# Kernel tuning notes

Measured on AMD Instinct MI355X. Metric: run time of the kernel, lower is better.

Reference implementation:

```python
import jax, jax.numpy as jnp
import numpy as np

THRESHOLD = 0.95
B, T, H = 32, 2000, 512
NUM_TARGETS = 250.0  # alphas normalized so each row sums to this (mimics alpha *= num/_num)
MAX_LABEL_LEN = 256


def setup_inputs() -> dict:
    key = jax.random.key(0)
    k1, k2 = jax.random.split(key)
    hidden = jax.random.normal(k1, (B, T, H), dtype=jnp.float32)
    u = jax.random.uniform(k2, (B, T), dtype=jnp.float32)
    alphas = u / u.sum(-1, keepdims=True) * NUM_TARGETS  # per-row sum == NUM_TARGETS
    return {"hidden": hidden, "alphas": alphas, "max_label_len": MAX_LABEL_LEN}


def _cif(hidden, alphas, max_label_len, threshold=THRESHOLD):
    """Continuous integrate-and-fire: sequential scan over time + fire-gather."""
    Bn, Tn, Hn = hidden.shape

    def step(carry, inp):
        integrate, frame = carry              # [B], [B, H]
        alpha, h = inp                        # [B], [B, H]
        dist_completion = 1.0 - integrate
        integ = integrate + alpha
        fire = integ > threshold              # [B] bool
        cur = jnp.where(fire, dist_completion, alpha)
        remainds = alpha - cur
        frame_out = frame + cur[:, None] * h  # emitted frame at this step
        integ_next = jnp.where(fire, integ - 1.0, integ)
        frame_next = jnp.where(fire[:, None], remainds[:, None] * h, frame_out)
        return (integ_next, frame_next), (integ, frame_out)

    init = (jnp.zeros((Bn,), hidden.dtype), jnp.zeros((Bn, Hn), hidden.dtype))
    xs = (jnp.swapaxes(alphas, 0, 1), jnp.swapaxes(hidden, 0, 1))  # time-major
    _, (fires_t, frames_t) = jax.lax.scan(step, init, xs)
    fires = jnp.swapaxes(fires_t, 0, 1)    # [B, T]
    frames = jnp.swapaxes(frames_t, 0, 1)  # [B, T, H]

    # Gather fired frames per batch row, left-packed and zero-padded to max_label_len.
    mask = fires > threshold                               # [B, T]
    pos = jnp.cumsum(mask.astype(jnp.int32), axis=1) - 1   # running fire index
    pos = jnp.where(mask, pos, max_label_len)              # non-fires go to dump slot
    out = jnp.zeros((Bn, max_label_len + 1, Hn), hidden.dtype)
    out = out.at[jnp.arange(Bn)[:, None], pos].set(frames)
    return out[:, :max_label_len]  # drop dump slot -> [B, L, H]


def reference(hidden, alphas, max_label_len):
    return _cif(hidden, alphas, max_label_len)
```

## Files before the change

### kernel.cpp

```cpp
#include <hip/hip_runtime.h>
#include <stdint.h>

static constexpr int   Bn      = 32;
static constexpr int   Tn      = 2000;
static constexpr int   Hn      = 512;
static constexpr int   Ln      = 256;
static constexpr float kThresh = 0.95f;
static constexpr int   TCHUNK  = 40;
static constexpr int   NTCH    = Tn / TCHUNK;
static constexpr int   CSPLIT  = 2;
static constexpr int   MSTRIDE = 64;
static constexpr unsigned PUBF = 0x40000000u;

__global__ __launch_bounds__(64, 1) void cif_fused_kernel(
    const float* __restrict__ hidden,
    const float* __restrict__ alphas,
    uint64_t* __restrict__ meta,
    float* __restrict__ out) {
  const int lane = threadIdx.x;
  __shared__ __align__(16) float alds[Tn + 64];

  if (blockIdx.x < Bn) {
    __builtin_amdgcn_s_setprio(3);
    const int b = blockIdx.x;
    {
      const float4* __restrict__ arow =
          reinterpret_cast<const float4*>(alphas + (size_t)b * Tn);
      for (int i = lane; i < Tn / 4; i += 64)
        *reinterpret_cast<float4*>(&alds[4 * i]) = arow[i];
      for (int i = Tn / 4 + lane; i < (Tn + 64) / 4; i += 64)
        *reinterpret_cast<float4*>(&alds[4 * i]) =
            make_float4(0.f, 0.f, 0.f, 0.f);
    }
    __syncthreads();

    const float4* __restrict__ lds4 =
        reinterpret_cast<const float4*>(&alds[0]);
    float I  = 0.0f;
    int   fc = 0;

    float4 q0 = lds4[0], q1 = lds4[1], q2 = lds4[2], q3 = lds4[3],
           q4 = lds4[4];
    int rd = 5;

    auto step4 = [&](const float4& q) {
#pragma unroll
      for (int j = 0; j < 4; ++j) {
        const float a = (j == 0) ? q.x : (j == 1) ? q.y : (j == 2) ? q.z : q.w;
        const float integ = I + a;
        const bool  fire  = integ > kThresh;
        I  = fire ? (integ - 1.0f) : integ;
        fc += fire ? 1 : 0;
      }
    };

    for (int c = 0; c < 100; ++c) {
      if (lane == 0 && (c & 1) == 0) {
        const uint64_t v = ((uint64_t)__float_as_uint(I) << 32) |
                           (uint64_t)(PUBF | (unsigned)fc);
        __hip_atomic_store(&meta[(size_t)b * MSTRIDE + (c >> 1)], v,
                           __ATOMIC_RELAXED, __HIP_MEMORY_SCOPE_AGENT);
      }
      step4(q0); q0 = lds4[rd + 0];
      step4(q1); q1 = lds4[rd + 1];
      step4(q2); q2 = lds4[rd + 2];
      step4(q3); q3 = lds4[rd + 3];
      step4(q4); q4 = lds4[rd + 4];
      rd += 5;
    }
    return;
  }

  const int idx  = blockIdx.x - Bn;
  const int b    = idx & (Bn - 1);
  const int q    = idx >> 5;
  const int tc   = q >> 1;
  const int half = q & 1;
  const int t_start = tc * TCHUNK;
  const int col  = half * (Hn / CSPLIT) + lane * 4;

  auto wait_meta = [&](int c) -> uint64_t {
    const uint64_t* p = &meta[(size_t)b * MSTRIDE + c];
    uint64_t v;
    for (;;) {
      v = __hip_atomic_load(p, __ATOMIC_RELAXED, __HIP_MEMORY_SCOPE_AGENT);
      if ((unsigned)v & PUBF) break;
      __builtin_amdgcn_s_sleep(16);
    }
    return v;
  };

  const float* __restrict__ arow = alphas + (size_t)b * Tn;

  float I; int s;
  if (tc == 0) { I = 0.0f; s = 0; }
  else {
    const uint64_t v = wait_meta(tc);
    I = __uint_as_float((unsigned)(v >> 32));
    s = (int)((unsigned)v & 0xFFFFu);
  }

  int   t_prev   = -1;
  float rem_prev = 0.0f;
  for (int k = 1; tc - k >= 0 && t_prev < 0; ++k) {
    const int ck = tc - k;
    float Ik;
    if (ck == 0) Ik = 0.0f;
    else {
      const uint64_t v = wait_meta(ck);
      Ik = __uint_as_float((unsigned)(v >> 32));
    }
    const float* __restrict__ ap = arow + ck * TCHUNK;
    int lt = -1; float lrem = 0.0f;
#pragma unroll
    for (int j = 0; j < TCHUNK; ++j) {
      const float a     = ap[j];
      const float integ = Ik + a;
      const bool  fire  = integ > kThresh;
      if (fire) { lt = ck * TCHUNK + j; lrem = a - (1.0f - Ik); }
      Ik = fire ? (integ - 1.0f) : integ;
    }
    if (lt >= 0) { t_prev = lt; rem_prev = lrem; }
  }

  const float* __restrict__ hb = hidden + (size_t)b * Tn * Hn + col;
  float4 acc = make_float4(0.f, 0.f, 0.f, 0.f);

  auto loadh = [&](int t) -> float4 {
    return *reinterpret_cast<const float4*>(hb + (size_t)t * Hn);
  };

  if (t_prev >= 0) {
    const float4 h = loadh(t_prev);
    acc.x = rem_prev * h.x; acc.y = rem_prev * h.y;
    acc.z = rem_prev * h.z; acc.w = rem_prev * h.w;
  }
  for (int t = t_prev + 1; t < t_start; ++t) {
    const float a  = arow[t];
    const float4 h = loadh(t);
    acc.x += a * h.x; acc.y += a * h.y;
    acc.z += a * h.z; acc.w += a * h.w;
  }

  float4 hc = loadh(t_start);
  for (int j = 0; j < TCHUNK; ++j) {
    const int t  = t_start + j;
    const int tn = (j + 1 < TCHUNK) ? t + 1 : t;
    const float4 hn = loadh(tn);
    const float a     = arow[t];
    const float integ = I + a;
    const bool  fire  = integ > kThresh;
    if (fire) {
      const float cw = 1.0f - I;
      acc.x += cw * hc.x; acc.y += cw * hc.y;
      acc.z += cw * hc.z; acc.w += cw * hc.w;
      if (s < Ln) {
        float* op = out + ((size_t)b * Ln + s) * Hn + col;
        *reinterpret_cast<float4*>(op) = acc;
      }
      const float rem = a - cw;
      acc.x = rem * hc.x; acc.y = rem * hc.y;
      acc.z = rem * hc.z; acc.w = rem * hc.w;
      s += 1;
      I  = integ - 1.0f;
    } else {
      acc.x += a * hc.x; acc.y += a * hc.y;
      acc.z += a * hc.z; acc.w += a * hc.w;
      I = integ;
    }
    hc = hn;
  }
  if (tc == NTCH - 1) {
    const float4 z = make_float4(0.f, 0.f, 0.f, 0.f);
    for (int s2 = s; s2 < Ln; ++s2) {
      float* op = out + ((size_t)b * Ln + s2) * Hn + col;
      *reinterpret_cast<float4*>(op) = z;
    }
  }
}

extern "C" void kernel_launch(void* const* d_in, const int* in_sizes, int n_in,
                              void* d_out, int out_size, void* d_ws, size_t ws_size,
                              hipStream_t stream) {
  const float* hidden = (const float*)d_in[0];
  const float* alphas = (const float*)d_in[1];
  float* out = (float*)d_out;

  uint64_t* meta = (uint64_t*)d_ws;
  hipMemsetAsync(meta, 0, (size_t)Bn * MSTRIDE * sizeof(uint64_t), stream);

  const int nblocks = Bn + NTCH * Bn * CSPLIT;
  cif_fused_kernel<<<nblocks, 64, 0, stream>>>(hidden, alphas, meta, out);
}
```

Measured before the change: 56.43 us.

## Split hidden columns four ways and deepen prefetch of hidden rows

```diff
diff --git a/kernel.cpp b/kernel.cpp
--- a/kernel.cpp
+++ b/kernel.cpp
@@ -8,7 +8,7 @@
 static constexpr float kThresh = 0.95f;
 static constexpr int   TCHUNK  = 40;
 static constexpr int   NTCH    = Tn / TCHUNK;
-static constexpr int   CSPLIT  = 2;
+static constexpr int   CSPLIT  = 4;
 static constexpr int   MSTRIDE = 64;
 static constexpr unsigned PUBF = 0x40000000u;
 
@@ -74,10 +74,10 @@
   const int idx  = blockIdx.x - Bn;
   const int b    = idx & (Bn - 1);
   const int q    = idx >> 5;
-  const int tc   = q >> 1;
-  const int half = q & 1;
+  const int tc   = q >> 2;
+  const int quar = q & 3;
   const int t_start = tc * TCHUNK;
-  const int col  = half * (Hn / CSPLIT) + lane * 4;
+  const int col  = quar * (Hn / CSPLIT) + lane * 2;
 
   auto wait_meta = [&](int c) -> uint64_t {
     const uint64_t* p = &meta[(size_t)b * MSTRIDE + c];
@@ -124,57 +124,55 @@
   }
 
   const float* __restrict__ hb = hidden + (size_t)b * Tn * Hn + col;
-  float4 acc = make_float4(0.f, 0.f, 0.f, 0.f);
+  float2 acc = make_float2(0.f, 0.f);
 
-  auto loadh = [&](int t) -> float4 {
-    return *reinterpret_cast<const float4*>(hb + (size_t)t * Hn);
+  auto loadh = [&](int t) -> float2 {
+    return *reinterpret_cast<const float2*>(hb + (size_t)t * Hn);
   };
 
   if (t_prev >= 0) {
-    const float4 h = loadh(t_prev);
+    const float2 h = loadh(t_prev);
     acc.x = rem_prev * h.x; acc.y = rem_prev * h.y;
-    acc.z = rem_prev * h.z; acc.w = rem_prev * h.w;
   }
   for (int t = t_prev + 1; t < t_start; ++t) {
     const float a  = arow[t];
-    const float4 h = loadh(t);
+    const float2 h = loadh(t);
     acc.x += a * h.x; acc.y += a * h.y;
-    acc.z += a * h.z; acc.w += a * h.w;
   }
 
-  float4 hc = loadh(t_start);
+  float2 p0 = loadh(t_start);
+  float2 p1 = loadh(t_start + 1);
+  float2 p2 = loadh(t_start + 2);
+  float2 p3 = loadh(t_start + 3);
   for (int j = 0; j < TCHUNK; ++j) {
-    const int t  = t_start + j;
-    const int tn = (j + 1 < TCHUNK) ? t + 1 : t;
-    const float4 hn = loadh(tn);
+    const int t   = t_start + j;
+    const int tpf = t_start + ((j + 4 < TCHUNK) ? j + 4 : TCHUNK - 1);
+    const float2 pn = loadh(tpf);
     const float a     = arow[t];
     const float integ = I + a;
     const bool  fire  = integ > kThresh;
     if (fire) {
       const float cw = 1.0f - I;
-      acc.x += cw * hc.x; acc.y += cw * hc.y;
-      acc.z += cw * hc.z; acc.w += cw * hc.w;
+      acc.x += cw * p0.x; acc.y += cw * p0.y;
       if (s < Ln) {
         float* op = out + ((size_t)b * Ln + s) * Hn + col;
-        *reinterpret_cast<float4*>(op) = acc;
+        *reinterpret_cast<float2*>(op) = acc;
       }
       const float rem = a - cw;
-      acc.x = rem * hc.x; acc.y = rem * hc.y;
-      acc.z = rem * hc.z; acc.w = rem * hc.w;
+      acc.x = rem * p0.x; acc.y = rem * p0.y;
       s += 1;
       I  = integ - 1.0f;
     } else {
-      acc.x += a * hc.x; acc.y += a * hc.y;
-      acc.z += a * hc.z; acc.w += a * hc.w;
+      acc.x += a * p0.x; acc.y += a * p0.y;
       I = integ;
     }
-    hc = hn;
+    p0 = p1; p1 = p2; p2 = p3; p3 = pn;
   }
   if (tc == NTCH - 1) {
-    const float4 z = make_float4(0.f, 0.f, 0.f, 0.f);
+    const float2 z = make_float2(0.f, 0.f);
     for (int s2 = s; s2 < Ln; ++s2) {
       float* op = out + ((size_t)b * Ln + s2) * Hn + col;
-      *reinterpret_cast<float4*>(op) = z;
+      *reinterpret_cast<float2*>(op) = z;
     }
   }
 }
```

Result: no change. 56.71 us (+0.5%).

## Publish last-fire position per chunk and skip trailing non-firing work

Applied to the files above, without the earlier changes.

```diff
diff --git a/kernel.cpp b/kernel.cpp
--- a/kernel.cpp
+++ b/kernel.cpp
@@ -16,6 +16,7 @@
     const float* __restrict__ hidden,
     const float* __restrict__ alphas,
     uint64_t* __restrict__ meta,
+    uint64_t* __restrict__ meta2,
     float* __restrict__ out) {
   const int lane = threadIdx.x;
   __shared__ __align__(16) float alds[Tn + 64];
@@ -36,19 +37,24 @@
 
     const float4* __restrict__ lds4 =
         reinterpret_cast<const float4*>(&alds[0]);
-    float I  = 0.0f;
-    int   fc = 0;
+    float I       = 0.0f;
+    int   fc      = 0;
+    int   lastT1  = 0;
+    float lastRem = 0.0f;
 
     float4 q0 = lds4[0], q1 = lds4[1], q2 = lds4[2], q3 = lds4[3],
            q4 = lds4[4];
     int rd = 5;
 
-    auto step4 = [&](const float4& q) {
+    auto step4 = [&](const float4& q, int tbase) {
 #pragma unroll
       for (int j = 0; j < 4; ++j) {
         const float a = (j == 0) ? q.x : (j == 1) ? q.y : (j == 2) ? q.z : q.w;
         const float integ = I + a;
         const bool  fire  = integ > kThresh;
+        const float cw    = 1.0f - I;
+        lastT1  = fire ? (tbase + j + 1) : lastT1;
+        lastRem = fire ? (a - cw) : lastRem;
         I  = fire ? (integ - 1.0f) : integ;
         fc += fire ? 1 : 0;
       }
@@ -56,16 +62,21 @@
 
     for (int c = 0; c < 100; ++c) {
       if (lane == 0 && (c & 1) == 0) {
-        const uint64_t v = ((uint64_t)__float_as_uint(I) << 32) |
-                           (uint64_t)(PUBF | (unsigned)fc);
-        __hip_atomic_store(&meta[(size_t)b * MSTRIDE + (c >> 1)], v,
+        const uint64_t v1 = ((uint64_t)__float_as_uint(I) << 32) |
+                            (uint64_t)(PUBF | (unsigned)fc);
+        __hip_atomic_store(&meta[(size_t)b * MSTRIDE + (c >> 1)], v1,
+                           __ATOMIC_RELAXED, __HIP_MEMORY_SCOPE_AGENT);
+        const uint64_t v2 = ((uint64_t)__float_as_uint(lastRem) << 32) |
+                            (uint64_t)(PUBF | (unsigned)lastT1);
+        __hip_atomic_store(&meta2[(size_t)b * MSTRIDE + (c >> 1)], v2,
                            __ATOMIC_RELAXED, __HIP_MEMORY_SCOPE_AGENT);
       }
-      step4(q0); q0 = lds4[rd + 0];
-      step4(q1); q1 = lds4[rd + 1];
-      step4(q2); q2 = lds4[rd + 2];
-      step4(q3); q3 = lds4[rd + 3];
-      step4(q4); q4 = lds4[rd + 4];
+      const int t0 = c * 20;
+      step4(q0, t0);      q0 = lds4[rd + 0];
+      step4(q1, t0 + 4);  q1 = lds4[rd + 1];
+      step4(q2, t0 + 8);  q2 = lds4[rd + 2];
+      step4(q3, t0 + 12); q3 = lds4[rd + 3];
+      step4(q4, t0 + 16); q4 = lds4[rd + 4];
       rd += 5;
     }
     return;
@@ -79,8 +90,8 @@
   const int t_start = tc * TCHUNK;
   const int col  = half * (Hn / CSPLIT) + lane * 4;
 
-  auto wait_meta = [&](int c) -> uint64_t {
-    const uint64_t* p = &meta[(size_t)b * MSTRIDE + c];
+  auto wait64 = [&](uint64_t* arr, int c) -> uint64_t {
+    const uint64_t* p = &arr[(size_t)b * MSTRIDE + c];
     uint64_t v;
     for (;;) {
       v = __hip_atomic_load(p, __ATOMIC_RELAXED, __HIP_MEMORY_SCOPE_AGENT);
@@ -95,41 +106,50 @@
   float I; int s;
   if (tc == 0) { I = 0.0f; s = 0; }
   else {
-    const uint64_t v = wait_meta(tc);
+    const uint64_t v = wait64(meta, tc);
     I = __uint_as_float((unsigned)(v >> 32));
     s = (int)((unsigned)v & 0xFFFFu);
   }
 
-  int   t_prev   = -1;
-  float rem_prev = 0.0f;
-  for (int k = 1; tc - k >= 0 && t_prev < 0; ++k) {
-    const int ck = tc - k;
-    float Ik;
-    if (ck == 0) Ik = 0.0f;
-    else {
-      const uint64_t v = wait_meta(ck);
-      Ik = __uint_as_float((unsigned)(v >> 32));
-    }
-    const float* __restrict__ ap = arow + ck * TCHUNK;
-    int lt = -1; float lrem = 0.0f;
+  float* __restrict__ const obase = out + (size_t)b * Ln * Hn + col;
+
+  int jlast = -1, nf = 0;
+  {
+    float Ip = I;
 #pragma unroll
     for (int j = 0; j < TCHUNK; ++j) {
-      const float a     = ap[j];
-      const float integ = Ik + a;
+      const float a     = arow[t_start + j];
+      const float integ = Ip + a;
       const bool  fire  = integ > kThresh;
-      if (fire) { lt = ck * TCHUNK + j; lrem = a - (1.0f - Ik); }
-      Ik = fire ? (integ - 1.0f) : integ;
-    }
-    if (lt >= 0) { t_prev = lt; rem_prev = lrem; }
+      jlast = fire ? j : jlast;
+      nf   += fire ? 1 : 0;
+      Ip = fire ? (integ - 1.0f) : integ;
+    }
+  }
+
+  if (jlast < 0) {
+    if (tc == NTCH - 1) {
+      const float4 z = make_float4(0.f, 0.f, 0.f, 0.f);
+      for (int s2 = (s < Ln ? s : Ln); s2 < Ln; ++s2)
+        *reinterpret_cast<float4*>(obase + (size_t)s2 * Hn) = z;
+    }
+    return;
+  }
+
+  int   t_prev; float rem_prev;
+  if (tc == 0) { t_prev = -1; rem_prev = 0.0f; }
+  else {
+    const uint64_t v2 = wait64(meta2, tc);
+    t_prev   = (int)((unsigned)v2 & 0x7FFu) - 1;
+    rem_prev = __uint_as_float((unsigned)(v2 >> 32));
   }
 
   const float* __restrict__ hb = hidden + (size_t)b * Tn * Hn + col;
-  float4 acc = make_float4(0.f, 0.f, 0.f, 0.f);
-
   auto loadh = [&](int t) -> float4 {
     return *reinterpret_cast<const float4*>(hb + (size_t)t * Hn);
   };
 
+  float4 acc = make_float4(0.f, 0.f, 0.f, 0.f);
   if (t_prev >= 0) {
     const float4 h = loadh(t_prev);
     acc.x = rem_prev * h.x; acc.y = rem_prev * h.y;
@@ -143,10 +163,10 @@
   }
 
   float4 hc = loadh(t_start);
-  for (int j = 0; j < TCHUNK; ++j) {
+  for (int j = 0; j <= jlast; ++j) {
     const int t  = t_start + j;
-    const int tn = (j + 1 < TCHUNK) ? t + 1 : t;
-    const float4 hn = loadh(tn);
+    const int jn = (j + 1 <= jlast) ? j + 1 : jlast;
+    const float4 hn = loadh(t_start + jn);
     const float a     = arow[t];
     const float integ = I + a;
     const bool  fire  = integ > kThresh;
@@ -154,10 +174,8 @@
       const float cw = 1.0f - I;
       acc.x += cw * hc.x; acc.y += cw * hc.y;
       acc.z += cw * hc.z; acc.w += cw * hc.w;
-      if (s < Ln) {
-        float* op = out + ((size_t)b * Ln + s) * Hn + col;
-        *reinterpret_cast<float4*>(op) = acc;
-      }
+      if (s < Ln)
+        *reinterpret_cast<float4*>(obase + (size_t)s * Hn) = acc;
       const float rem = a - cw;
       acc.x = rem * hc.x; acc.y = rem * hc.y;
       acc.z = rem * hc.z; acc.w = rem * hc.w;
@@ -172,10 +190,8 @@
   }
   if (tc == NTCH - 1) {
     const float4 z = make_float4(0.f, 0.f, 0.f, 0.f);
-    for (int s2 = s; s2 < Ln; ++s2) {
-      float* op = out + ((size_t)b * Ln + s2) * Hn + col;
-      *reinterpret_cast<float4*>(op) = z;
-    }
+    for (int s2 = (s < Ln ? s : Ln); s2 < Ln; ++s2)
+      *reinterpret_cast<float4*>(obase + (size_t)s2 * Hn) = z;
   }
 }
 
@@ -186,9 +202,11 @@
   const float* alphas = (const float*)d_in[1];
   float* out = (float*)d_out;
 
-  uint64_t* meta = (uint64_t*)d_ws;
-  hipMemsetAsync(meta, 0, (size_t)Bn * MSTRIDE * sizeof(uint64_t), stream);
+  uint64_t* meta  = (uint64_t*)d_ws;
+  uint64_t* meta2 = meta + (size_t)Bn * MSTRIDE;
+  hipMemsetAsync(meta, 0, (size_t)Bn * MSTRIDE * 2 * sizeof(uint64_t), stream);
 
   const int nblocks = Bn + NTCH * Bn * CSPLIT;
-  cif_fused_kernel<<<nblocks, 64, 0, stream>>>(hidden, alphas, meta, out);
+  cif_fused_kernel<<<nblocks, 64, 0, stream>>>(hidden, alphas, meta, meta2,
+                                               out);
 }
```

Measured after the change: 88.74 us. 57.3% more time.
